# Optimization experiments

Measured on AMD Instinct MI355X. Metric: run time of the kernel, lower is better.

Reference implementation:

```python
import jax, jax.numpy as jnp
import numpy as np


def setup_inputs() -> dict:
    key = jax.random.key(0)
    kx, kb, kc, ka = jax.random.split(key, 4)
    batch, seq_len, state_dim = 4, 4096, 1024
    shape = (batch, seq_len, state_dim)
    x = jax.random.normal(kx, shape, dtype=jnp.float32)
    B = jax.random.normal(kb, shape, dtype=jnp.float32)
    C = jax.random.normal(kc, shape, dtype=jnp.float32)
    A = jax.random.uniform(ka, shape, dtype=jnp.float32)  # decay gates in (0,1)
    return {"x": x, "B": B, "C": C, "A": A}


def reference(x, B, C, A):
    # Diagonal selective-scan recurrence: h_t = A_t * h_{t-1} + B_t; y_t = C_t * h_t.
    # x is accepted for interface parity but unused (as in the original module).
    # Scan over time with carry h: [batch, state_dim].
    A_t = jnp.moveaxis(A, 1, 0)  # [seq, batch, dim]
    B_t = jnp.moveaxis(B, 1, 0)
    C_t = jnp.moveaxis(C, 1, 0)
    h0 = jnp.zeros((B.shape[0], B.shape[2]), dtype=B.dtype)

    def step(h, abc):
        a, b, c = abc
        h = a * h + b
        return h, c * h

    _, ys = jax.lax.scan(step, h0, (A_t, B_t, C_t))
    return jnp.moveaxis(ys, 0, 1)  # [batch, seq, dim]
```

## Files before the change

kernel.cpp:

```cpp
#include <hip/hip_runtime.h>

#define BATCH 4
#define SEQ   4096
#define DIM   1024
#define DIM4  (DIM / 4)
#define NC    512
#define CHUNK (SEQ / NC)

__device__ __forceinline__ float4 f4_fma(float4 a, float4 h, float4 b) {
    float4 r;
    r.x = fmaf(a.x, h.x, b.x);
    r.y = fmaf(a.y, h.y, b.y);
    r.z = fmaf(a.z, h.z, b.z);
    r.w = fmaf(a.w, h.w, b.w);
    return r;
}

__device__ __forceinline__ float4 f4_mul(float4 a, float4 b) {
    float4 r;
    r.x = a.x * b.x;
    r.y = a.y * b.y;
    r.z = a.z * b.z;
    r.w = a.w * b.w;
    return r;
}

__global__ __launch_bounds__(256) void ssm_phase1(const float4* __restrict__ A,
                                                  const float4* __restrict__ B,
                                                  float4* __restrict__ P,
                                                  float4* __restrict__ Q) {
    const int c  = blockIdx.x % NC;
    const int b  = blockIdx.x / NC;
    const int d4 = threadIdx.x;

    size_t base = ((size_t)b * SEQ + (size_t)c * CHUNK) * DIM4 + d4;

    float4 p = make_float4(1.f, 1.f, 1.f, 1.f);
    float4 q = make_float4(0.f, 0.f, 0.f, 0.f);

#pragma unroll
    for (int t = 0; t < CHUNK; ++t) {
        float4 a  = A[base + (size_t)t * DIM4];
        float4 bb = B[base + (size_t)t * DIM4];
        q = f4_fma(a, q, bb);
        p = f4_mul(p, a);
    }

    size_t w = ((size_t)b * NC + c) * DIM4 + d4;
    P[w] = p;
    Q[w] = q;
}

__global__ __launch_bounds__(NC) void ssm_phase2(float4* __restrict__ PH,
                                                 const float4* __restrict__ Q) {
    const int b  = blockIdx.x / DIM4;
    const int d4 = blockIdx.x % DIM4;
    const int c  = threadIdx.x;

    __shared__ float4 sp[NC];
    __shared__ float4 sq[NC];

    const size_t idx = ((size_t)b * NC + c) * DIM4 + d4;
    float4 p = PH[idx];
    float4 q = Q[idx];
    sp[c] = p;
    sq[c] = q;
    __syncthreads();

    for (int off = 1; off < NC; off <<= 1) {
        float4 pp, qq;
        const bool has = (c >= off);
        if (has) { pp = sp[c - off]; qq = sq[c - off]; }
        __syncthreads();
        if (has) {
            q = f4_fma(p, qq, q);
            p = f4_mul(p, pp);
            sp[c] = p;
            sq[c] = q;
        }
        __syncthreads();
    }

    float4 h = (c == 0) ? make_float4(0.f, 0.f, 0.f, 0.f) : sq[c - 1];
    PH[idx] = h;
}

__global__ __launch_bounds__(256) void ssm_phase3(const float4* __restrict__ A,
                                                  const float4* __restrict__ B,
                                                  const float4* __restrict__ C,
                                                  const float4* __restrict__ H,
                                                  float4* __restrict__ Y) {
    const int c  = blockIdx.x % NC;
    const int b  = blockIdx.x / NC;
    const int d4 = threadIdx.x;

    size_t base = ((size_t)b * SEQ + (size_t)c * CHUNK) * DIM4 + d4;

    float4 h = H[((size_t)b * NC + c) * DIM4 + d4];

#pragma unroll
    for (int t = 0; t < CHUNK; ++t) {
        float4 a  = A[base + (size_t)t * DIM4];
        float4 bb = B[base + (size_t)t * DIM4];
        float4 cc = C[base + (size_t)t * DIM4];
        h = f4_fma(a, h, bb);
        Y[base + (size_t)t * DIM4] = f4_mul(cc, h);
    }
}

extern "C" void kernel_launch(void* const* d_in, const int* in_sizes, int n_in,
                              void* d_out, int out_size, void* d_ws, size_t ws_size,
                              hipStream_t stream) {
    const float* B = (const float*)d_in[1];
    const float* C = (const float*)d_in[2];
    const float* A = (const float*)d_in[3];
    float* Y = (float*)d_out;

    float* P = (float*)d_ws;
    float* Q = P + (size_t)BATCH * NC * DIM;

    ssm_phase1<<<BATCH * NC, 256, 0, stream>>>(
        (const float4*)A, (const float4*)B, (float4*)P, (float4*)Q);

    ssm_phase2<<<BATCH * DIM4, NC, 0, stream>>>(
        (float4*)P, (const float4*)Q);

    ssm_phase3<<<BATCH * NC, 256, 0, stream>>>(
        (const float4*)A, (const float4*)B, (const float4*)C,
        (const float4*)P, (float4*)Y);
}
```

Before: 95.29 us.

## Software-pipeline chunk loads across four chunks per block in phases 1 and 3

Each block of phases 1 and 3 now handles four consecutive chunks instead of one. It double-buffers register arrays so the loads for the next chunk are issued before the current chunk is computed, and uses empty asm statements to keep the loaded values pinned in registers. Phase 3 also writes its output with nontemporal stores. The aim is to raise memory-level parallelism per thread and hide load latency. The cost is four times fewer blocks, higher register pressure, and launch_bounds(256,1) occupancy hints.

```diff
diff --git a/kernel.cpp b/kernel.cpp
--- a/kernel.cpp
+++ b/kernel.cpp
@@ -6,9 +6,13 @@
 #define DIM4  (DIM / 4)
 #define NC    512
 #define CHUNK (SEQ / NC)
+#define SLOTS 4
+#define BPB   (NC / SLOTS)
 
-__device__ __forceinline__ float4 f4_fma(float4 a, float4 h, float4 b) {
-    float4 r;
+typedef float vf4 __attribute__((ext_vector_type(4)));
+
+__device__ __forceinline__ vf4 vfma4(vf4 a, vf4 h, vf4 b) {
+    vf4 r;
     r.x = fmaf(a.x, h.x, b.x);
     r.y = fmaf(a.y, h.y, b.y);
     r.z = fmaf(a.z, h.z, b.z);
@@ -16,116 +20,152 @@
     return r;
 }
 
-__device__ __forceinline__ float4 f4_mul(float4 a, float4 b) {
-    float4 r;
-    r.x = a.x * b.x;
-    r.y = a.y * b.y;
-    r.z = a.z * b.z;
-    r.w = a.w * b.w;
-    return r;
+__global__ __launch_bounds__(256, 1) void ssm_phase1(const vf4* __restrict__ gA,
+                                                     const vf4* __restrict__ gB,
+                                                     vf4* __restrict__ gP,
+                                                     vf4* __restrict__ gQ) {
+    const int j  = blockIdx.x;
+    const int b  = j / BPB;
+    const int c0 = (j % BPB) * SLOTS;
+    const int d4 = threadIdx.x;
+
+#define P1BASE(s) (((size_t)b * SEQ + (size_t)(c0 + (s)) * CHUNK) * DIM4 + d4)
+
+#define P1LOAD(av, bv, s) do { const size_t _sb = P1BASE(s);                              \
+    _Pragma("unroll") for (int t = 0; t < CHUNK; ++t) { av[t] = gA[_sb + (size_t)t * DIM4]; } \
+    _Pragma("unroll") for (int t = 0; t < CHUNK; ++t) { bv[t] = gB[_sb + (size_t)t * DIM4]; } \
+  } while (0)
+
+#define PIN16(av, bv) asm volatile("" :                                                    \
+    "+v"(av[0]), "+v"(av[1]), "+v"(av[2]), "+v"(av[3]),                                    \
+    "+v"(av[4]), "+v"(av[5]), "+v"(av[6]), "+v"(av[7]),                                    \
+    "+v"(bv[0]), "+v"(bv[1]), "+v"(bv[2]), "+v"(bv[3]),                                    \
+    "+v"(bv[4]), "+v"(bv[5]), "+v"(bv[6]), "+v"(bv[7]))
+
+#define P1COMP(av, bv, s) do {                                                             \
+    vf4 p = av[0], q = bv[0];                                                              \
+    _Pragma("unroll") for (int t = 1; t < CHUNK; ++t) { q = vfma4(av[t], q, bv[t]); p = p * av[t]; } \
+    const size_t _w = ((size_t)b * NC + (size_t)(c0 + (s))) * DIM4 + d4;                   \
+    gP[_w] = p; gQ[_w] = q;                                                                \
+  } while (0)
+
+    vf4 a0[CHUNK], b0[CHUNK], a1[CHUNK], b1[CHUNK];
+
+    P1LOAD(a0, b0, 0);
+    P1LOAD(a1, b1, 1);
+    PIN16(a0, b0);  P1COMP(a0, b0, 0);
+    P1LOAD(a0, b0, 2);
+    PIN16(a1, b1);  P1COMP(a1, b1, 1);
+    P1LOAD(a1, b1, 3);
+    PIN16(a0, b0);  P1COMP(a0, b0, 2);
+    PIN16(a1, b1);  P1COMP(a1, b1, 3);
+
+#undef P1BASE
+#undef P1LOAD
+#undef PIN16
+#undef P1COMP
 }
 
-__global__ __launch_bounds__(256) void ssm_phase1(const float4* __restrict__ A,
-                                                  const float4* __restrict__ B,
-                                                  float4* __restrict__ P,
-                                                  float4* __restrict__ Q) {
-    const int c  = blockIdx.x % NC;
-    const int b  = blockIdx.x / NC;
-    const int d4 = threadIdx.x;
-
-    size_t base = ((size_t)b * SEQ + (size_t)c * CHUNK) * DIM4 + d4;
-
-    float4 p = make_float4(1.f, 1.f, 1.f, 1.f);
-    float4 q = make_float4(0.f, 0.f, 0.f, 0.f);
-
-#pragma unroll
-    for (int t = 0; t < CHUNK; ++t) {
-        float4 a  = A[base + (size_t)t * DIM4];
-        float4 bb = B[base + (size_t)t * DIM4];
-        q = f4_fma(a, q, bb);
-        p = f4_mul(p, a);
-    }
-
-    size_t w = ((size_t)b * NC + c) * DIM4 + d4;
-    P[w] = p;
-    Q[w] = q;
-}
-
-__global__ __launch_bounds__(NC) void ssm_phase2(float4* __restrict__ PH,
-                                                 const float4* __restrict__ Q) {
+__global__ __launch_bounds__(NC) void ssm_phase2(vf4* __restrict__ PH,
+                                                 const vf4* __restrict__ Q) {
     const int b  = blockIdx.x / DIM4;
     const int d4 = blockIdx.x % DIM4;
     const int c  = threadIdx.x;
 
-    __shared__ float4 sp[NC];
-    __shared__ float4 sq[NC];
+    __shared__ vf4 sp[NC];
+    __shared__ vf4 sq[NC];
 
     const size_t idx = ((size_t)b * NC + c) * DIM4 + d4;
-    float4 p = PH[idx];
-    float4 q = Q[idx];
+    vf4 p = PH[idx];
+    vf4 q = Q[idx];
     sp[c] = p;
     sq[c] = q;
     __syncthreads();
 
     for (int off = 1; off < NC; off <<= 1) {
-        float4 pp, qq;
+        vf4 pp, qq;
         const bool has = (c >= off);
         if (has) { pp = sp[c - off]; qq = sq[c - off]; }
         __syncthreads();
         if (has) {
-            q = f4_fma(p, qq, q);
-            p = f4_mul(p, pp);
+            q = vfma4(p, qq, q);
+            p = p * pp;
             sp[c] = p;
             sq[c] = q;
         }
         __syncthreads();
     }
 
-    float4 h = (c == 0) ? make_float4(0.f, 0.f, 0.f, 0.f) : sq[c - 1];
+    vf4 h = (c == 0) ? (vf4)(0.f) : sq[c - 1];
     PH[idx] = h;
 }
 
-__global__ __launch_bounds__(256) void ssm_phase3(const float4* __restrict__ A,
-                                                  const float4* __restrict__ B,
-                                                  const float4* __restrict__ C,
-                                                  const float4* __restrict__ H,
-                                                  float4* __restrict__ Y) {
-    const int c  = blockIdx.x % NC;
-    const int b  = blockIdx.x / NC;
+__global__ __launch_bounds__(256, 1) void ssm_phase3(const vf4* __restrict__ gA,
+                                                     const vf4* __restrict__ gB,
+                                                     const vf4* __restrict__ gC,
+                                                     const vf4* __restrict__ gH,
+                                                     vf4* __restrict__ gY) {
+    const int j  = blockIdx.x;
+    const int b  = j / BPB;
+    const int c0 = (j % BPB) * SLOTS;
     const int d4 = threadIdx.x;
 
-    size_t base = ((size_t)b * SEQ + (size_t)c * CHUNK) * DIM4 + d4;
+#define P3BASE(s) (((size_t)b * SEQ + (size_t)(c0 + (s)) * CHUNK) * DIM4 + d4)
 
-    float4 h = H[((size_t)b * NC + c) * DIM4 + d4];
+#define P3LOAD(av, bv, cv, hh, s) do { const size_t _sb = P3BASE(s);                       \
+    _Pragma("unroll") for (int t = 0; t < CHUNK; ++t) { av[t] = gA[_sb + (size_t)t * DIM4]; } \
+    _Pragma("unroll") for (int t = 0; t < CHUNK; ++t) { bv[t] = gB[_sb + (size_t)t * DIM4]; } \
+    _Pragma("unroll") for (int t = 0; t < CHUNK; ++t) { cv[t] = gC[_sb + (size_t)t * DIM4]; } \
+    hh = gH[((size_t)b * NC + (size_t)(c0 + (s))) * DIM4 + d4];                            \
+  } while (0)
 
-#pragma unroll
-    for (int t = 0; t < CHUNK; ++t) {
-        float4 a  = A[base + (size_t)t * DIM4];
-        float4 bb = B[base + (size_t)t * DIM4];
-        float4 cc = C[base + (size_t)t * DIM4];
-        h = f4_fma(a, h, bb);
-        Y[base + (size_t)t * DIM4] = f4_mul(cc, h);
-    }
+#define PIN25(av, bv, cv, hh) asm volatile("" :                                            \
+    "+v"(av[0]), "+v"(av[1]), "+v"(av[2]), "+v"(av[3]),                                    \
+    "+v"(av[4]), "+v"(av[5]), "+v"(av[6]), "+v"(av[7]),                                    \
+    "+v"(bv[0]), "+v"(bv[1]), "+v"(bv[2]), "+v"(bv[3]),                                    \
+    "+v"(bv[4]), "+v"(bv[5]), "+v"(bv[6]), "+v"(bv[7]),                                    \
+    "+v"(cv[0]), "+v"(cv[1]), "+v"(cv[2]), "+v"(cv[3]),                                    \
+    "+v"(cv[4]), "+v"(cv[5]), "+v"(cv[6]), "+v"(cv[7]),                                    \
+    "+v"(hh))
+
+#define P3COMP(av, bv, cv, hh, s) do { const size_t _sb = P3BASE(s); vf4 h = hh;           \
+    _Pragma("unroll") for (int t = 0; t < CHUNK; ++t) {                                    \
+        h = vfma4(av[t], h, bv[t]);                                                        \
+        __builtin_nontemporal_store(cv[t] * h, &gY[_sb + (size_t)t * DIM4]);               \
+    } } while (0)
+
+    vf4 a0[CHUNK], b0[CHUNK], cc0[CHUNK], h0;
+    vf4 a1[CHUNK], b1[CHUNK], cc1[CHUNK], h1;
+
+    P3LOAD(a0, b0, cc0, h0, 0);
+    P3LOAD(a1, b1, cc1, h1, 1);
+    PIN25(a0, b0, cc0, h0);  P3COMP(a0, b0, cc0, h0, 0);
+    P3LOAD(a0, b0, cc0, h0, 2);
+    PIN25(a1, b1, cc1, h1);  P3COMP(a1, b1, cc1, h1, 1);
+    P3LOAD(a1, b1, cc1, h1, 3);
+    PIN25(a0, b0, cc0, h0);  P3COMP(a0, b0, cc0, h0, 2);
+    PIN25(a1, b1, cc1, h1);  P3COMP(a1, b1, cc1, h1, 3);
+
+#undef P3BASE
+#undef P3LOAD
+#undef PIN25
+#undef P3COMP
 }
 
 extern "C" void kernel_launch(void* const* d_in, const int* in_sizes, int n_in,
                               void* d_out, int out_size, void* d_ws, size_t ws_size,
                               hipStream_t stream) {
-    const float* B = (const float*)d_in[1];
-    const float* C = (const float*)d_in[2];
-    const float* A = (const float*)d_in[3];
-    float* Y = (float*)d_out;
+    const vf4* B = (const vf4*)d_in[1];
+    const vf4* C = (const vf4*)d_in[2];
+    const vf4* A = (const vf4*)d_in[3];
+    vf4* Y = (vf4*)d_out;
 
-    float* P = (float*)d_ws;
-    float* Q = P + (size_t)BATCH * NC * DIM;
+    vf4* P = (vf4*)d_ws;
+    vf4* Q = P + (size_t)BATCH * NC * DIM4;
 
-    ssm_phase1<<<BATCH * NC, 256, 0, stream>>>(
-        (const float4*)A, (const float4*)B, (float4*)P, (float4*)Q);
+    ssm_phase1<<<BATCH * BPB, 256, 0, stream>>>(A, B, P, Q);
 
-    ssm_phase2<<<BATCH * DIM4, NC, 0, stream>>>(
-        (float4*)P, (const float4*)Q);
+    ssm_phase2<<<BATCH * DIM4, NC, 0, stream>>>(P, Q);
 
-    ssm_phase3<<<BATCH * NC, 256, 0, stream>>>(
-        (const float4*)A, (const float4*)B, (const float4*)C,
-        (const float4*)P, (float4*)Y);
+    ssm_phase3<<<BATCH * BPB, 256, 0, stream>>>(A, B, C, P, Y);
 }
```

After: 94.82 us. No clear change (-0.5%).
